# Performance work log

Hardware: AMD Instinct MI355X
Metric: run time of the kernel (lower is better)

The kernel has to match this reference:

```python
import jax, jax.numpy as jnp
import numpy as np

DIM = 512
HEADS = 8
HEAD_DIM = DIM // HEADS
SCALE = HEAD_DIM ** -0.5
CPB_HIDDEN = 512
N_CLASSES = 2
LN_EPS = 1e-5


def _layernorm(x, g, b):
    m = jnp.mean(x, axis=-1, keepdims=True)
    v = jnp.var(x, axis=-1, keepdims=True)
    return (x - m) / jnp.sqrt(v + LN_EPS) * g + b


def _coord_attention(x, coords, cpb_w1, cpb_b1, cpb_w2, cpb_b2, qkv_w, qkv_b, proj_w, proj_b):
    B, N, C = x.shape
    qkv = (x @ qkv_w + qkv_b).reshape(B, N, 3, HEADS, HEAD_DIM)
    q, k, v = jnp.moveaxis(qkv, 2, 0)  # each (B, N, H, hd)
    attn = jnp.einsum('bnhd,bmhd->bhnm', q * SCALE, k)  # (B, H, N, N)
    rel = coords[:, :, None, :] - coords[:, None, :, :]  # (B, N, N, 2)
    rel = rel / (jnp.linalg.norm(rel, axis=-1, keepdims=True) + 1e-6)
    bias = jax.nn.relu(rel @ cpb_w1 + cpb_b1) @ cpb_w2 + cpb_b2  # (B, N, N, H)
    attn = jax.nn.softmax(attn + jnp.transpose(bias, (0, 3, 1, 2)), axis=-1)
    out = jnp.einsum('bhnm,bmhd->bnhd', attn, v).reshape(B, N, C)
    return out @ proj_w + proj_b


def setup_inputs() -> dict:
    key = jax.random.key(0)
    ks = iter(jax.random.split(key, 32))
    d = {}
    d['h'] = jax.random.normal(next(ks), (1, 400, 1024), dtype=jnp.float32)
    d['coords'] = jax.random.uniform(next(ks), (1, 400, 2), dtype=jnp.float32) * 1000.0
    def lin(kw, kb, fan_in, fan_out):
        w = jax.random.normal(kw, (fan_in, fan_out), dtype=jnp.float32) / np.sqrt(fan_in)
        b = jax.random.normal(kb, (fan_out,), dtype=jnp.float32) * 0.01
        return w, b
    d['fc1_w'], d['fc1_b'] = lin(next(ks), next(ks), 1024, DIM)
    d['cls_token'] = jax.random.normal(next(ks), (1, 1, DIM), dtype=jnp.float32)
    for p in ('l1', 'l2'):
        d[p + '_norm_g'] = jnp.ones((DIM,), jnp.float32)
        d[p + '_norm_b'] = jnp.zeros((DIM,), jnp.float32)
        d[p + '_cpb_w1'], d[p + '_cpb_b1'] = lin(next(ks), next(ks), 2, CPB_HIDDEN)
        d[p + '_cpb_w2'], d[p + '_cpb_b2'] = lin(next(ks), next(ks), CPB_HIDDEN, HEADS)
        d[p + '_qkv_w'], d[p + '_qkv_b'] = lin(next(ks), next(ks), DIM, 3 * DIM)
        d[p + '_proj_w'], d[p + '_proj_b'] = lin(next(ks), next(ks), DIM, DIM)
    d['norm_g'] = jnp.ones((DIM,), jnp.float32)
    d['norm_b'] = jnp.zeros((DIM,), jnp.float32)
    d['fc2_w'], d['fc2_b'] = lin(next(ks), next(ks), DIM, N_CLASSES)
    return d


def reference(h, coords, fc1_w, fc1_b, cls_token,
              l1_norm_g, l1_norm_b, l1_cpb_w1, l1_cpb_b1, l1_cpb_w2, l1_cpb_b2,
              l1_qkv_w, l1_qkv_b, l1_proj_w, l1_proj_b,
              l2_norm_g, l2_norm_b, l2_cpb_w1, l2_cpb_b1, l2_cpb_w2, l2_cpb_b2,
              l2_qkv_w, l2_qkv_b, l2_proj_w, l2_proj_b,
              norm_g, norm_b, fc2_w, fc2_b):
    B, Np, _ = h.shape
    h = jax.nn.relu(h @ fc1_w + fc1_b)  # (B, N, 512)
    side = int(np.ceil(np.sqrt(Np)))
    add = side * side - Np  # pad bag to a perfect square (wrap-around copy)
    h = jnp.concatenate([h, h[:, :add, :]], axis=1)
    coords = jnp.concatenate([coords, coords[:, :add, :]], axis=1)
    cls = jnp.broadcast_to(cls_token, (B, 1, DIM))
    h = jnp.concatenate([cls, h], axis=1)
    coords = jnp.concatenate([jnp.zeros((B, 1, 2), h.dtype), coords], axis=1)
    h = h + _coord_attention(_layernorm(h, l1_norm_g, l1_norm_b), coords,
                             l1_cpb_w1, l1_cpb_b1, l1_cpb_w2, l1_cpb_b2,
                             l1_qkv_w, l1_qkv_b, l1_proj_w, l1_proj_b)
    h = h + _coord_attention(_layernorm(h, l2_norm_g, l2_norm_b), coords,
                             l2_cpb_w1, l2_cpb_b1, l2_cpb_w2, l2_cpb_b2,
                             l2_qkv_w, l2_qkv_b, l2_proj_w, l2_proj_b)
    h = _layernorm(h, norm_g, norm_b)[:, 0]  # CLS token
    return h @ fc2_w + fc2_b  # (B, n_classes)
```

## Files before the change

### kernel.cpp

```cpp
#include <hip/hip_runtime.h>
#include <math.h>

#define NP 401
#define DIM 512
#define LN_EPS 1e-5f
#define ATT_SCALE 0.125f
#define SP 448
#define PLANE (NP * SP)
#define CPB_M 4096
#define TSTRIDE (CPB_M + 64)
#define PQS (401L * 1536)
#define PKS (401L * 1024)
#define PVS (401L * 512)

template<bool TB, typename LA, typename LB>
__device__ __forceinline__ void gemm64(
    int kBeg, int kEnd, int tid,
    float (*as)[68], float (*bs)[68], float (&acc)[4][4],
    LA&& loadA, LB&& loadB)
{
    float aR[4], bR[4];
    loadA(kBeg, aR);
    loadB(kBeg, bR);
    for (int k0 = kBeg; k0 < kEnd; k0 += 16) {
        const int arow = tid >> 2, aq = tid & 3;
        as[aq * 4 + 0][arow] = aR[0];
        as[aq * 4 + 1][arow] = aR[1];
        as[aq * 4 + 2][arow] = aR[2];
        as[aq * 4 + 3][arow] = aR[3];
        if (!TB) {
            *(float4*)&bs[tid >> 4][(tid & 15) * 4] =
                make_float4(bR[0], bR[1], bR[2], bR[3]);
        } else {
            bs[aq * 4 + 0][arow] = bR[0];
            bs[aq * 4 + 1][arow] = bR[1];
            bs[aq * 4 + 2][arow] = bR[2];
            bs[aq * 4 + 3][arow] = bR[3];
        }
        __syncthreads();
        float nA[4] = {0.f,0.f,0.f,0.f}, nB[4] = {0.f,0.f,0.f,0.f};
        if (k0 + 16 < kEnd) { loadA(k0 + 16, nA); loadB(k0 + 16, nB); }
        const int tx = tid & 15, ty = tid >> 4;
        #pragma unroll
        for (int kk = 0; kk < 16; ++kk) {
            float4 a4 = *(const float4*)&as[kk][ty * 4];
            float4 b4 = *(const float4*)&bs[kk][tx * 4];
            float av[4] = {a4.x, a4.y, a4.z, a4.w};
            float bv[4] = {b4.x, b4.y, b4.z, b4.w};
            #pragma unroll
            for (int r = 0; r < 4; ++r)
                #pragma unroll
                for (int c = 0; c < 4; ++c)
                    acc[r][c] = fmaf(av[r], bv[c], acc[r][c]);
        }
        __syncthreads();
        #pragma unroll
        for (int j = 0; j < 4; ++j) { aR[j] = nA[j]; bR[j] = nB[j]; }
    }
}

__global__ __launch_bounds__(256) void gemm_split_kernel(
    const float* __restrict__ A, int lda,
    const float* __restrict__ B, int ldb,
    float* __restrict__ P, int ldc, long slice,
    int M, int N, int K, int skN)
{
    __shared__ float as[16][68], bs[16][68];
    const int tid = threadIdx.x;
    const int m0 = blockIdx.x * 64, n0 = blockIdx.y * 64;
    const int sk = blockIdx.z;
    const int KS = ((K + skN * 16 - 1) / (skN * 16)) * 16;
    const int kBeg = sk * KS;
    const int kEnd = (kBeg + KS < K) ? kBeg + KS : K;
    float acc[4][4] = {};

    auto loadA = [&](int k0, float r[4]) {
        r[0] = r[1] = r[2] = r[3] = 0.f;
        int gm = m0 + (tid >> 2);
        if (gm >= M) return;
        int gk = k0 + (tid & 3) * 4;
        const float* p = A + (long)gm * lda + gk;
        if (gk + 3 < kEnd) {
            float4 v = *(const float4*)p;
            r[0] = v.x; r[1] = v.y; r[2] = v.z; r[3] = v.w;
        } else {
            #pragma unroll
            for (int j = 0; j < 4; ++j) if (gk + j < kEnd) r[j] = p[j];
        }
    };
    auto loadB = [&](int k0, float r[4]) {
        r[0] = r[1] = r[2] = r[3] = 0.f;
        int gk = k0 + (tid >> 4);
        if (gk >= kEnd) return;
        int gn = n0 + (tid & 15) * 4;
        const float* p = B + (long)gk * ldb + gn;
        float4 v = *(const float4*)p;
        r[0] = v.x; r[1] = v.y; r[2] = v.z; r[3] = v.w;
    };
    if (kBeg < kEnd)
        gemm64<false>(kBeg, kEnd, tid, as, bs, acc, loadA, loadB);

    float* C = P + (long)sk * slice;
    const int tx = tid & 15, ty = tid >> 4;
    #pragma unroll
    for (int r = 0; r < 4; ++r) {
        int m = m0 + ty * 4 + r;
        if (m >= M) continue;
        *(float4*)&C[(long)m * ldc + n0 + tx * 4] =
            make_float4(acc[r][0], acc[r][1], acc[r][2], acc[r][3]);
    }
}

__global__ __launch_bounds__(256) void reduce_kernel(
    const float* __restrict__ P, long slice, int skN,
    const float* __restrict__ bias, float* __restrict__ out,
    int total, int N)
{
    int idx = (blockIdx.x * 256 + threadIdx.x) * 4;
    if (idx >= total) return;
    float4 s = *(const float4*)(P + idx);
    for (int k = 1; k < skN; ++k) {
        float4 p = *(const float4*)(P + (long)k * slice + idx);
        s.x += p.x; s.y += p.y; s.z += p.z; s.w += p.w;
    }
    if (bias) {
        const float4 b = *(const float4*)(bias + (idx % N));
        s.x += b.x; s.y += b.y; s.z += b.z; s.w += b.w;
    }
    *(float4*)(out + idx) = s;
}

__global__ __launch_bounds__(256) void qk_kernel(
    const float* __restrict__ qkv,
    const int* __restrict__ pm, const float* __restrict__ pf,
    const float* __restrict__ T, float* __restrict__ S,
    float* __restrict__ Sml)
{
    __shared__ float as[16][68], bs[16][68];
    const int tid = threadIdx.x;
    const int m0 = blockIdx.x * 64, n0 = blockIdx.y * 64, h = blockIdx.z;
    const int nb = blockIdx.y;
    float acc[4][4] = {};

    auto loadQ = [&](int k0, float r[4]) {
        int gm = m0 + (tid >> 2);
        if (gm > 400) { r[0]=r[1]=r[2]=r[3]=0.f; return; }
        int gk = k0 + (tid & 3) * 4;
        float4 v = *(const float4*)(qkv + (long)gm * 1536 + h * 64 + gk);
        r[0]=v.x; r[1]=v.y; r[2]=v.z; r[3]=v.w;
    };
    auto loadK = [&](int k0, float r[4]) {
        int gn = n0 + (tid >> 2);
        if (gn > 400) { r[0]=r[1]=r[2]=r[3]=0.f; return; }
        int gk = k0 + (tid & 3) * 4;
        float4 v = *(const float4*)(qkv + (long)gn * 1536 + 512 + h * 64 + gk);
        r[0]=v.x; r[1]=v.y; r[2]=v.z; r[3]=v.w;
    };
    gemm64<true>(0, 64, tid, as, bs, acc, loadQ, loadK);

    const int tx = tid & 15, ty = tid >> 4;
    const float* Tt = T + (long)h * TSTRIDE;
    float* Sp = S + (long)h * PLANE;
    #pragma unroll
    for (int r = 0; r < 4; ++r) {
        int i = m0 + ty * 4 + r;
        float sv[4];
        #pragma unroll
        for (int c = 0; c < 4; ++c) {
            int j = n0 + tx * 4 + c;
            if (i <= 400 && j <= 400) {
                int id = i * 416 + j;
                int mm = pm[id];
                float fr = pf[id];
                float t0 = Tt[mm], t1 = Tt[mm + 1];
                sv[c] = fmaf(acc[r][c], ATT_SCALE, fmaf(fr, t1 - t0, t0));
                Sp[(long)i * SP + j] = sv[c];
            } else {
                sv[c] = -INFINITY;
            }
        }
        float cmax = fmaxf(fmaxf(sv[0], sv[1]), fmaxf(sv[2], sv[3]));
        cmax = fmaxf(cmax, __shfl_xor(cmax, 1));
        cmax = fmaxf(cmax, __shfl_xor(cmax, 2));
        cmax = fmaxf(cmax, __shfl_xor(cmax, 4));
        cmax = fmaxf(cmax, __shfl_xor(cmax, 8));
        float cs = __expf(sv[0] - cmax) + __expf(sv[1] - cmax)
                 + __expf(sv[2] - cmax) + __expf(sv[3] - cmax);
        cs += __shfl_xor(cs, 1);
        cs += __shfl_xor(cs, 2);
        cs += __shfl_xor(cs, 4);
        cs += __shfl_xor(cs, 8);
        if (tx == 0 && i <= 400) {
            long o = ((long)(h * 401 + i) * 7 + nb) * 2;
            Sml[o] = cmax;
            Sml[o + 1] = cs;
        }
    }
}

__global__ __launch_bounds__(256) void pv_kernel(
    const float* __restrict__ S, const float* __restrict__ Sml,
    const float* __restrict__ qkv, float* __restrict__ Pv)
{
    __shared__ float as[16][68], bs[16][68];
    __shared__ float rml[64][2];
    const int tid = threadIdx.x;
    const int m0 = blockIdx.x * 64;
    const int h = blockIdx.z >> 2, sk = blockIdx.z & 3;
    const int kBeg = sk * 112;
    const int kEnd = (kBeg + 112 < NP) ? kBeg + 112 : NP;
    float acc[4][4] = {};

    if (tid < 64) {
        int row = m0 + tid;
        float M = -INFINITY, L = 0.f;
        if (row <= 400) {
            const float* q = Sml + ((long)(h * 401 + row) * 7) * 2;
            #pragma unroll
            for (int c = 0; c < 7; ++c) M = fmaxf(M, q[c * 2]);
            #pragma unroll
            for (int c = 0; c < 7; ++c) L += q[c * 2 + 1] * __expf(q[c * 2] - M);
        }
        rml[tid][0] = M;
        rml[tid][1] = (L > 0.f) ? (1.f / L) : 0.f;
    }
    __syncthreads();

    auto loadA = [&](int k0, float r[4]) {
        int gm = m0 + (tid >> 2);
        if (gm > 400) { r[0]=r[1]=r[2]=r[3]=0.f; return; }
        float M = rml[tid >> 2][0], IL = rml[tid >> 2][1];
        int gk = k0 + (tid & 3) * 4;
        const float* p = S + (long)h * PLANE + (long)gm * SP + gk;
        float t4[4] = {-INFINITY, -INFINITY, -INFINITY, -INFINITY};
        if (gk + 3 < kEnd) {
            float4 v = *(const float4*)p;
            t4[0]=v.x; t4[1]=v.y; t4[2]=v.z; t4[3]=v.w;
        } else {
            #pragma unroll
            for (int j = 0; j < 4; ++j) if (gk + j < kEnd) t4[j] = p[j];
        }
        #pragma unroll
        for (int j = 0; j < 4; ++j) r[j] = __expf(t4[j] - M) * IL;
    };
    auto loadB = [&](int k0, float r[4]) {
        r[0] = r[1] = r[2] = r[3] = 0.f;
        int key = k0 + (tid >> 4);
        if (key >= kEnd) return;
        int d = (tid & 15) * 4;
        float4 v = *(const float4*)(qkv + (long)key * 1536 + 1024 + h * 64 + d);
        r[0]=v.x; r[1]=v.y; r[2]=v.z; r[3]=v.w;
    };
    gemm64<false>(kBeg, kEnd, tid, as, bs, acc, loadA, loadB);

    float* C = Pv + (long)sk * PVS;
    const int tx = tid & 15, ty = tid >> 4;
    #pragma unroll
    for (int r = 0; r < 4; ++r) {
        int m = m0 + ty * 4 + r;
        if (m > 400) continue;
        *(float4*)&C[(long)m * 512 + h * 64 + tx * 4] =
            make_float4(acc[r][0], acc[r][1], acc[r][2], acc[r][3]);
    }
}

__global__ __launch_bounds__(256) void proj_kernel(
    const float* __restrict__ att, const float* __restrict__ projw,
    float* __restrict__ Pp)
{
    __shared__ float as[16][68], bs[16][68];
    const int tid = threadIdx.x;
    const int m0 = blockIdx.x * 64, n0 = blockIdx.y * 64, sk = blockIdx.z;
    const int kBeg = sk * 64, kEnd = kBeg + 64;
    float acc[4][4] = {};

    auto loadA = [&](int k0, float r[4]) {
        r[0] = r[1] = r[2] = r[3] = 0.f;
        int gm = m0 + (tid >> 2);
        if (gm > 400) return;
        int gk = k0 + (tid & 3) * 4;
        float4 v = *(const float4*)(att + (long)gm * 512 + gk);
        r[0]=v.x; r[1]=v.y; r[2]=v.z; r[3]=v.w;
    };
    auto loadB = [&](int k0, float r[4]) {
        int gk = k0 + (tid >> 4);
        int gn = n0 + (tid & 15) * 4;
        float4 v = *(const float4*)(projw + (long)gk * 512 + gn);
        r[0]=v.x; r[1]=v.y; r[2]=v.z; r[3]=v.w;
    };
    gemm64<false>(kBeg, kEnd, tid, as, bs, acc, loadA, loadB);

    float* C = Pp + (long)sk * PVS;
    const int tx = tid & 15, ty = tid >> 4;
    #pragma unroll
    for (int r = 0; r < 4; ++r) {
        int m = m0 + ty * 4 + r;
        if (m > 400) continue;
        *(float4*)&C[(long)m * 512 + n0 + tx * 4] =
            make_float4(acc[r][0], acc[r][1], acc[r][2], acc[r][3]);
    }
}

__global__ __launch_bounds__(256) void rowfuse_kernel(
    const float* __restrict__ P, long slice, int skN, int rowOff,
    const float* __restrict__ bias, int doRelu,
    const float* __restrict__ resid, const float* __restrict__ cls,
    float* __restrict__ h0,
    const float* __restrict__ g, const float* __restrict__ b,
    float* __restrict__ xln)
{
    const int r = blockIdx.x, t = threadIdx.x;
    float v0, v1;
    if (cls && r == 0) {
        v0 = cls[t]; v1 = cls[t + 256];
    } else {
        const float* p = P + (long)(r - rowOff) * DIM;
        v0 = bias[t]; v1 = bias[t + 256];
        for (int k = 0; k < skN; ++k) {
            v0 += p[(long)k * slice + t];
            v1 += p[(long)k * slice + t + 256];
        }
        if (resid) {
            v0 += resid[(long)r * DIM + t];
            v1 += resid[(long)r * DIM + t + 256];
        }
        if (doRelu) { v0 = fmaxf(v0, 0.f); v1 = fmaxf(v1, 0.f); }
    }
    h0[(long)r * DIM + t] = v0;
    h0[(long)r * DIM + t + 256] = v1;

    float s = v0 + v1, sq = v0 * v0 + v1 * v1;
    #pragma unroll
    for (int off = 32; off > 0; off >>= 1) {
        s += __shfl_down(s, off);
        sq += __shfl_down(sq, off);
    }
    __shared__ float ps[4], pq[4];
    int w = t >> 6, lane = t & 63;
    if (lane == 0) { ps[w] = s; pq[w] = sq; }
    __syncthreads();
    float Sm = ps[0] + ps[1] + ps[2] + ps[3];
    float Q = pq[0] + pq[1] + pq[2] + pq[3];
    float mean = Sm * (1.f / DIM);
    float var = Q * (1.f / DIM) - mean * mean;
    float inv = rsqrtf(var + LN_EPS);
    xln[(long)r * DIM + t]       = (v0 - mean) * inv * g[t] + b[t];
    xln[(long)r * DIM + t + 256] = (v1 - mean) * inv * g[t + 256] + b[t + 256];
}

__global__ __launch_bounds__(256) void cls_decode_kernel(
    const float* __restrict__ xln, const float* __restrict__ qkvw,
    const float* __restrict__ Pkv, const float* __restrict__ qkvb,
    const int* __restrict__ pm, const float* __restrict__ pf,
    const float* __restrict__ T,
    float* __restrict__ cms, float* __restrict__ cpv,
    unsigned* __restrict__ cnt)
{
    const int h = blockIdx.x, c = blockIdx.y, tid = threadIdx.x;
    const int kBeg = c * 64;
    __shared__ float q0[64], scraw[64], p[64], red[4][64], rr[2];

    if (h == 0 && c == 0 && tid == 0) *cnt = 0u;

    {
        int d = tid & 63, w4 = tid >> 6;
        const float* col = qkvw + h * 64 + d;
        float acc = 0.f;
        for (int k = w4 * 128; k < w4 * 128 + 128; ++k)
            acc = fmaf(xln[k], col[(long)k * 1536], acc);
        red[w4][d] = acc;
    }
    __syncthreads();
    if (tid < 64)
        q0[tid] = red[0][tid] + red[1][tid] + red[2][tid] + red[3][tid]
                  + qkvb[h * 64 + tid];
    __syncthreads();

    {
        int k = tid >> 2, q = tid & 3;
        int j = kBeg + k;
        float dot = 0.f;
        if (j < NP) {
            long base = (long)j * 1024 + h * 64 + q * 16;
            #pragma unroll
            for (int d = 0; d < 16; d += 4) {
                float4 x0 = *(const float4*)(Pkv + base + d);
                float4 x1 = *(const float4*)(Pkv + PKS + base + d);
                float4 x2 = *(const float4*)(Pkv + 2 * PKS + base + d);
                float4 x3 = *(const float4*)(Pkv + 3 * PKS + base + d);
                float4 bb = *(const float4*)(qkvb + 512 + h * 64 + q * 16 + d);
                float4 qq = *(const float4*)(q0 + q * 16 + d);
                dot = fmaf(qq.x, x0.x + x1.x + x2.x + x3.x + bb.x, dot);
                dot = fmaf(qq.y, x0.y + x1.y + x2.y + x3.y + bb.y, dot);
                dot = fmaf(qq.z, x0.z + x1.z + x2.z + x3.z + bb.z, dot);
                dot = fmaf(qq.w, x0.w + x1.w + x2.w + x3.w + bb.w, dot);
            }
        }
        dot += __shfl_down(dot, 2);
        dot += __shfl_down(dot, 1);
        if (q == 0) scraw[k] = dot;
    }
    __syncthreads();

    if (tid < 64) {
        int j = kBeg + tid;
        float s;
        if (j < NP) {
            int mm = pm[j];
            float fr = pf[j];
            const float* Tt = T + (long)h * TSTRIDE;
            float t0 = Tt[mm], t1 = Tt[mm + 1];
            s = fmaf(scraw[tid], ATT_SCALE, fmaf(fr, t1 - t0, t0));
        } else {
            s = -INFINITY;
        }
        float m = s;
        #pragma unroll
        for (int off = 32; off > 0; off >>= 1)
            m = fmaxf(m, __shfl_xor(m, off));
        float e = (j < NP) ? __expf(s - m) : 0.f;
        float sum = e;
        #pragma unroll
        for (int off = 32; off > 0; off >>= 1)
            sum += __shfl_xor(sum, off);
        p[tid] = e;
        if (tid == 0) { rr[0] = m; rr[1] = sum; }
    }
    __syncthreads();

    {
        int w = tid >> 6, d = tid & 63;
        float vb = qkvb[1024 + h * 64 + d];
        float acc = 0.f;
        for (int k = w; k < 64; k += 4) {
            int j = kBeg + k;
            if (j >= NP) break;
            long o = (long)j * 1024 + 512 + h * 64 + d;
            float v = Pkv[o] + Pkv[PKS + o] + Pkv[2 * PKS + o]
                      + Pkv[3 * PKS + o] + vb;
            acc = fmaf(p[k], v, acc);
        }
        red[w][d] = acc;
    }
    __syncthreads();
    if (tid < 64) {
        cpv[((long)h * 7 + c) * 64 + tid] =
            red[0][tid] + red[1][tid] + red[2][tid] + red[3][tid];
        if (tid == 0) {
            cms[(h * 7 + c) * 2 + 0] = rr[0];
            cms[(h * 7 + c) * 2 + 1] = rr[1];
        }
    }
}

__global__ __launch_bounds__(256) void cls_proj_kernel(
    const float* __restrict__ cms, const float* __restrict__ cpv,
    const float* __restrict__ projw, const float* __restrict__ projb,
    float* __restrict__ proj0,
    const float* __restrict__ h0,
    const float* __restrict__ g, const float* __restrict__ b,
    const float* __restrict__ fc2w, const float* __restrict__ fc2b,
    float* __restrict__ out, unsigned* __restrict__ cnt)
{
    __shared__ float av[512], red[4][64];
    __shared__ int isLast;
    const int bk = blockIdx.x, tid = threadIdx.x;
    for (int d = tid; d < 512; d += 256) {
        int h = d >> 6, dd = d & 63;
        float M = -INFINITY;
        #pragma unroll
        for (int c = 0; c < 7; ++c)
            M = fmaxf(M, cms[(h * 7 + c) * 2]);
        float Sx = 0.f, acc = 0.f;
        #pragma unroll
        for (int c = 0; c < 7; ++c) {
            float e = __expf(cms[(h * 7 + c) * 2] - M);
            Sx += cms[(h * 7 + c) * 2 + 1] * e;
            acc += cpv[((long)h * 7 + c) * 64 + dd] * e;
        }
        av[d] = acc / Sx;
    }
    __syncthreads();
    int gg = tid >> 6, n = bk * 64 + (tid & 63);
    float acc = 0.f;
    for (int k = gg * 128; k < gg * 128 + 128; ++k)
        acc = fmaf(av[k], projw[(long)k * 512 + n], acc);
    red[gg][tid & 63] = acc;
    __syncthreads();
    if (tid < 64)
        proj0[bk * 64 + tid] = red[0][tid] + red[1][tid] + red[2][tid]
                               + red[3][tid] + projb[bk * 64 + tid];

    __threadfence();
    if (tid == 0) isLast = (atomicAdd(cnt, 1u) == 7u);
    __syncthreads();
    if (!isLast) return;
    __threadfence();

    const int t = tid;
    float v0 = h0[t] + proj0[t];
    float v1 = h0[t + 256] + proj0[t + 256];
    float s = v0 + v1, sq = v0 * v0 + v1 * v1;
    #pragma unroll
    for (int off = 32; off > 0; off >>= 1) {
        s += __shfl_down(s, off);
        sq += __shfl_down(sq, off);
    }
    __shared__ float ps[4], pq[4], pc0[4], pc1[4];
    int w = t >> 6, lane = t & 63;
    if (lane == 0) { ps[w] = s; pq[w] = sq; }
    __syncthreads();
    float Sm = ps[0] + ps[1] + ps[2] + ps[3];
    float Q = pq[0] + pq[1] + pq[2] + pq[3];
    float mean = Sm * (1.f / DIM);
    float var = Q * (1.f / DIM) - mean * mean;
    float inv = rsqrtf(var + LN_EPS);
    float n0 = (v0 - mean) * inv * g[t] + b[t];
    float n1 = (v1 - mean) * inv * g[t + 256] + b[t + 256];
    float c0 = n0 * fc2w[t * 2]     + n1 * fc2w[(t + 256) * 2];
    float c1 = n0 * fc2w[t * 2 + 1] + n1 * fc2w[(t + 256) * 2 + 1];
    #pragma unroll
    for (int off = 32; off > 0; off >>= 1) {
        c0 += __shfl_down(c0, off);
        c1 += __shfl_down(c1, off);
    }
    if (lane == 0) { pc0[w] = c0; pc1[w] = c1; }
    __syncthreads();
    if (t == 0) {
        out[0] = pc0[0] + pc0[1] + pc0[2] + pc0[3] + fc2b[0];
        out[1] = pc1[0] + pc1[1] + pc1[2] + pc1[3] + fc2b[1];
    }
}

__global__ __launch_bounds__(256) void mega_kernel(
    const float* __restrict__ hin, const float* __restrict__ fc1_w,
    const float* __restrict__ w1_0, const float* __restrict__ b1_0,
    const float* __restrict__ w2_0, const float* __restrict__ b2_0,
    const float* __restrict__ w1_1, const float* __restrict__ b1_1,
    const float* __restrict__ w2_1, const float* __restrict__ b2_1,
    const float* __restrict__ coords,
    float* __restrict__ Pp, float* __restrict__ T,
    int* __restrict__ pm, float* __restrict__ pf)
{
    __shared__ float smem[2176];
    float (*as)[68] = (float(*)[68])smem;
    float (*bs)[68] = (float(*)[68])(smem + 1088);
    float (*red)[64][8] = (float(*)[64][8])smem;
    const int bid = blockIdx.x, tid = threadIdx.x;

    if (bid < 896) {
        int sk = bid / 56, rem = bid % 56;
        int m0 = (rem % 7) * 64, n0 = (rem / 7) * 64;
        int kBeg = sk * 64, kEnd = kBeg + 64;
        float acc[4][4] = {};
        auto loadA = [&](int k0, float r[4]) {
            r[0]=r[1]=r[2]=r[3]=0.f;
            int gm = m0 + (tid >> 2);
            if (gm >= 400) return;
            int gk = k0 + (tid & 3) * 4;
            float4 v = *(const float4*)(hin + (long)gm * 1024 + gk);
            r[0]=v.x; r[1]=v.y; r[2]=v.z; r[3]=v.w;
        };
        auto loadB = [&](int k0, float r[4]) {
            int gk = k0 + (tid >> 4);
            int gn = n0 + (tid & 15) * 4;
            float4 v = *(const float4*)(fc1_w + (long)gk * 512 + gn);
            r[0]=v.x; r[1]=v.y; r[2]=v.z; r[3]=v.w;
        };
        gemm64<false>(kBeg, kEnd, tid, as, bs, acc, loadA, loadB);
        float* C = Pp + (long)sk * PVS;
        const int tx = tid & 15, ty = tid >> 4;
        #pragma unroll
        for (int r = 0; r < 4; ++r) {
            int m = m0 + ty * 4 + r;
            if (m >= 400) continue;
            *(float4*)&C[(long)m * 512 + n0 + tx * 4] =
                make_float4(acc[r][0], acc[r][1], acc[r][2], acc[r][3]);
        }
    } else if (bid < 1026) {
        int tb = bid - 896;
        int z = tb / 65, ab = tb % 65;
        const float* w1 = z ? w1_1 : w1_0;
        const float* b1 = z ? b1_1 : b1_0;
        const float* w2 = z ? w2_1 : w2_0;
        const float* b2 = z ? b2_1 : b2_0;
        const int lane = tid & 63, wv = tid >> 6;
        float ca = 0.f, sa = 0.f;
        if (ab != 64) {
            float th = fmaf((float)(ab * 64 + lane),
                            (float)(2.0 * M_PI / CPB_M), -(float)M_PI);
            sincosf(th, &sa, &ca);
        } else if (lane == 0) {
            sincosf((float)M_PI, &sa, &ca);
        }
        float a8[8] = {};
        const int kbeg = wv * 128;
        #pragma unroll 4
        for (int k = kbeg; k < kbeg + 128; ++k) {
            float hk = fmaxf(fmaf(ca, w1[k],
                                  fmaf(sa, w1[512 + k], b1[k])), 0.f);
            #pragma unroll
            for (int h2 = 0; h2 < 8; ++h2)
                a8[h2] = fmaf(hk, w2[k * 8 + h2], a8[h2]);
        }
        #pragma unroll
        for (int h2 = 0; h2 < 8; ++h2) red[wv][lane][h2] = a8[h2];
        __syncthreads();
        if (tid < 64) {
            int aidx = ab * 64 + tid;
            if (aidx <= CPB_M + 1) {
                #pragma unroll
                for (int h2 = 0; h2 < 8; ++h2)
                    T[(long)(z * 8 + h2) * TSTRIDE + aidx] =
                        red[0][tid][h2] + red[1][tid][h2] +
                        red[2][tid][h2] + red[3][tid][h2] + b2[h2];
            }
        }
    } else {
        int p = (bid - 1026) * 256 + tid;
        if (p < NP * NP) {
            int i = p / NP, j = p - i * NP;
            float xi = (i == 0) ? 0.f : coords[(i - 1) * 2];
            float yi = (i == 0) ? 0.f : coords[(i - 1) * 2 + 1];
            float xj = (j == 0) ? 0.f : coords[(j - 1) * 2];
            float yj = (j == 0) ? 0.f : coords[(j - 1) * 2 + 1];
            float rx = xi - xj, ry = yi - yj;
            int mm; float fr;
            if (rx == 0.f && ry == 0.f) {
                mm = CPB_M + 1; fr = 0.f;
            } else {
                float x = (atan2f(ry, rx) + 3.14159265358979f)
                          * (float)(CPB_M / (2.0 * M_PI));
                int mi = (int)x;
                fr = x - (float)mi;
                mm = (mi >= CPB_M) ? mi - CPB_M : mi;
            }
            pm[i * 416 + j] = mm;
            pf[i * 416 + j] = fr;
        }
    }
}

extern "C" void kernel_launch(void* const* d_in, const int* in_sizes, int n_in,
                              void* d_out, int out_size, void* d_ws, size_t ws_size,
                              hipStream_t stream)
{
    const float* coords = (const float*)d_in[1];
    float* ws = (float*)d_ws;
    float* h0   = ws;                    ws += 401L * 512;
    float* xln  = ws;                    ws += 401L * 512;
    float* S    = ws;                    ws += 8L * PLANE;
    float* T    = ws;                    ws += 16L * TSTRIDE;
    int*   pm   = (int*)ws;              ws += 401L * 416;
    float* pf   = ws;                    ws += 401L * 416;
    float* Pq   = ws;                    ws += 4L * PQS;
    float* qkv  = ws;                    ws += 401L * 1536;
    float* Pv   = ws;                    ws += 4L * PVS;
    float* att  = ws;                    ws += 401L * 512;
    float* Pp   = ws;                    ws += 16L * PVS;
    float* proj0 = ws;                   ws += 512;
    float* cms  = ws;                    ws += 8L * 7 * 2;
    float* cpv  = ws;                    ws += 8L * 7 * 64;
    float* Sml  = ws;                    ws += 8L * 401 * 7 * 2;
    unsigned* cnt = (unsigned*)ws;       ws += 16;

    mega_kernel<<<1655, 256, 0, stream>>>(
        (const float*)d_in[0], (const float*)d_in[2],
        (const float*)d_in[7],  (const float*)d_in[8],
        (const float*)d_in[9],  (const float*)d_in[10],
        (const float*)d_in[17], (const float*)d_in[18],
        (const float*)d_in[19], (const float*)d_in[20],
        coords, Pp, T, pm, pf);

    rowfuse_kernel<<<401, 256, 0, stream>>>(
        Pp, PVS, 16, 1, (const float*)d_in[3], 1, nullptr,
        (const float*)d_in[4], h0,
        (const float*)d_in[5], (const float*)d_in[6], xln);

    gemm_split_kernel<<<dim3(7, 24, 4), 256, 0, stream>>>(
        xln, 512, (const float*)d_in[11], 1536, Pq, 1536, PQS,
        401, 1536, 512, 4);
    reduce_kernel<<<602, 256, 0, stream>>>(
        Pq, PQS, 4, (const float*)d_in[12], qkv, 401 * 1536, 1536);
    qk_kernel<<<dim3(7, 7, 8), 256, 0, stream>>>(qkv, pm, pf, T, S, Sml);
    pv_kernel<<<dim3(7, 1, 32), 256, 0, stream>>>(S, Sml, qkv, Pv);
    reduce_kernel<<<201, 256, 0, stream>>>(
        Pv, PVS, 4, nullptr, att, 401 * 512, 512);
    proj_kernel<<<dim3(7, 8, 8), 256, 0, stream>>>(
        att, (const float*)d_in[13], Pp);
    rowfuse_kernel<<<401, 256, 0, stream>>>(
        Pp, PVS, 8, 0, (const float*)d_in[14], 0, h0, nullptr, h0,
        (const float*)d_in[15], (const float*)d_in[16], xln);

    gemm_split_kernel<<<dim3(7, 16, 4), 256, 0, stream>>>(
        xln, 512, (const float*)d_in[21] + 512, 1536, Pq, 1024, PKS,
        401, 1024, 512, 4);
    cls_decode_kernel<<<dim3(8, 7), 256, 0, stream>>>(
        xln, (const float*)d_in[21], Pq, (const float*)d_in[22],
        pm, pf, T + 8L * TSTRIDE, cms, cpv, cnt);
    cls_proj_kernel<<<8, 256, 0, stream>>>(
        cms, cpv, (const float*)d_in[23], (const float*)d_in[24], proj0,
        h0, (const float*)d_in[25], (const float*)d_in[26],
        (const float*)d_in[27], (const float*)d_in[28], (float*)d_out, cnt);
}
```

Before: 244.1 us.

## Fuse QK, softmax and PV into split-key flash kernel, combine in proj

Merges the score, softmax and PV stages into one kernel per (query tile, key tile, head). It computes local exp-probabilities and multiplies them by the V tile in shared memory, writing per-key-block partial outputs with their row max and sum. The projection kernel then rescales and sums the seven partials while loading its A operand. This removes the full score-plane write and read, the separate PV kernel and a reduce launch. In exchange the projection kernel reads seven partial outputs per element, with some redundant reads across column tiles.

```diff
diff --git a/kernel.cpp b/kernel.cpp
--- a/kernel.cpp
+++ b/kernel.cpp
@@ -5,8 +5,6 @@
 #define DIM 512
 #define LN_EPS 1e-5f
 #define ATT_SCALE 0.125f
-#define SP 448
-#define PLANE (NP * SP)
 #define CPB_M 4096
 #define TSTRIDE (CPB_M + 64)
 #define PQS (401L * 1536)
@@ -130,17 +128,39 @@
     *(float4*)(out + idx) = s;
 }
 
-__global__ __launch_bounds__(256) void qk_kernel(
+__global__ __launch_bounds__(256) void flash_kernel(
     const float* __restrict__ qkv,
     const int* __restrict__ pm, const float* __restrict__ pf,
-    const float* __restrict__ T, float* __restrict__ S,
-    float* __restrict__ Sml)
+    const float* __restrict__ T,
+    float* __restrict__ PO,
+    float* __restrict__ Pml)
 {
     __shared__ float as[16][68], bs[16][68];
+    __shared__ float pT[64][68];
+    __shared__ float vs[64][68];
     const int tid = threadIdx.x;
-    const int m0 = blockIdx.x * 64, n0 = blockIdx.y * 64, h = blockIdx.z;
-    const int nb = blockIdx.y;
+    const int m0 = blockIdx.x * 64, nb = blockIdx.y, h = blockIdx.z;
+    const int n0 = nb * 64;
     float acc[4][4] = {};
+
+    float vreg[4][4];
+    {
+        int key = n0 + (tid >> 2);
+        int d0 = (tid & 3) * 16;
+        if (key <= 400) {
+            const float* p = qkv + (long)key * 1536 + 1024 + h * 64 + d0;
+            #pragma unroll
+            for (int i = 0; i < 4; ++i) {
+                float4 v = *(const float4*)(p + i * 4);
+                vreg[i][0] = v.x; vreg[i][1] = v.y;
+                vreg[i][2] = v.z; vreg[i][3] = v.w;
+            }
+        } else {
+            #pragma unroll
+            for (int i = 0; i < 4; ++i)
+                vreg[i][0] = vreg[i][1] = vreg[i][2] = vreg[i][3] = 0.f;
+        }
+    }
 
     auto loadQ = [&](int k0, float r[4]) {
         int gm = m0 + (tid >> 2);
@@ -158,9 +178,17 @@
     };
     gemm64<true>(0, 64, tid, as, bs, acc, loadQ, loadK);
 
+    {
+        int key = tid >> 2, d0 = (tid & 3) * 16;
+        #pragma unroll
+        for (int i = 0; i < 4; ++i)
+            *(float4*)&vs[key][d0 + i * 4] =
+                make_float4(vreg[i][0], vreg[i][1], vreg[i][2], vreg[i][3]);
+    }
+
     const int tx = tid & 15, ty = tid >> 4;
     const float* Tt = T + (long)h * TSTRIDE;
-    float* Sp = S + (long)h * PLANE;
+    float p[4][4];
     #pragma unroll
     for (int r = 0; r < 4; ++r) {
         int i = m0 + ty * 4 + r;
@@ -174,7 +202,6 @@
                 float fr = pf[id];
                 float t0 = Tt[mm], t1 = Tt[mm + 1];
                 sv[c] = fmaf(acc[r][c], ATT_SCALE, fmaf(fr, t1 - t0, t0));
-                Sp[(long)i * SP + j] = sv[c];
             } else {
                 sv[c] = -INFINITY;
             }
@@ -184,103 +211,96 @@
         cmax = fmaxf(cmax, __shfl_xor(cmax, 2));
         cmax = fmaxf(cmax, __shfl_xor(cmax, 4));
         cmax = fmaxf(cmax, __shfl_xor(cmax, 8));
-        float cs = __expf(sv[0] - cmax) + __expf(sv[1] - cmax)
-                 + __expf(sv[2] - cmax) + __expf(sv[3] - cmax);
+        const bool rowok = (i <= 400);
+        #pragma unroll
+        for (int c = 0; c < 4; ++c)
+            p[r][c] = rowok ? __expf(sv[c] - cmax) : 0.f;
+        float cs = p[r][0] + p[r][1] + p[r][2] + p[r][3];
         cs += __shfl_xor(cs, 1);
         cs += __shfl_xor(cs, 2);
         cs += __shfl_xor(cs, 4);
         cs += __shfl_xor(cs, 8);
-        if (tx == 0 && i <= 400) {
+        if (tx == 0 && rowok) {
             long o = ((long)(h * 401 + i) * 7 + nb) * 2;
-            Sml[o] = cmax;
-            Sml[o + 1] = cs;
-        }
-    }
-}
-
-__global__ __launch_bounds__(256) void pv_kernel(
-    const float* __restrict__ S, const float* __restrict__ Sml,
-    const float* __restrict__ qkv, float* __restrict__ Pv)
-{
-    __shared__ float as[16][68], bs[16][68];
-    __shared__ float rml[64][2];
-    const int tid = threadIdx.x;
-    const int m0 = blockIdx.x * 64;
-    const int h = blockIdx.z >> 2, sk = blockIdx.z & 3;
-    const int kBeg = sk * 112;
-    const int kEnd = (kBeg + 112 < NP) ? kBeg + 112 : NP;
-    float acc[4][4] = {};
-
-    if (tid < 64) {
-        int row = m0 + tid;
-        float M = -INFINITY, L = 0.f;
-        if (row <= 400) {
-            const float* q = Sml + ((long)(h * 401 + row) * 7) * 2;
-            #pragma unroll
-            for (int c = 0; c < 7; ++c) M = fmaxf(M, q[c * 2]);
-            #pragma unroll
-            for (int c = 0; c < 7; ++c) L += q[c * 2 + 1] * __expf(q[c * 2] - M);
-        }
-        rml[tid][0] = M;
-        rml[tid][1] = (L > 0.f) ? (1.f / L) : 0.f;
-    }
-    __syncthreads();
-
-    auto loadA = [&](int k0, float r[4]) {
-        int gm = m0 + (tid >> 2);
-        if (gm > 400) { r[0]=r[1]=r[2]=r[3]=0.f; return; }
-        float M = rml[tid >> 2][0], IL = rml[tid >> 2][1];
-        int gk = k0 + (tid & 3) * 4;
-        const float* p = S + (long)h * PLANE + (long)gm * SP + gk;
-        float t4[4] = {-INFINITY, -INFINITY, -INFINITY, -INFINITY};
-        if (gk + 3 < kEnd) {
-            float4 v = *(const float4*)p;
-            t4[0]=v.x; t4[1]=v.y; t4[2]=v.z; t4[3]=v.w;
-        } else {
-            #pragma unroll
-            for (int j = 0; j < 4; ++j) if (gk + j < kEnd) t4[j] = p[j];
-        }
-        #pragma unroll
-        for (int j = 0; j < 4; ++j) r[j] = __expf(t4[j] - M) * IL;
-    };
-    auto loadB = [&](int k0, float r[4]) {
-        r[0] = r[1] = r[2] = r[3] = 0.f;
-        int key = k0 + (tid >> 4);
-        if (key >= kEnd) return;
-        int d = (tid & 15) * 4;
-        float4 v = *(const float4*)(qkv + (long)key * 1536 + 1024 + h * 64 + d);
-        r[0]=v.x; r[1]=v.y; r[2]=v.z; r[3]=v.w;
-    };
-    gemm64<false>(kBeg, kEnd, tid, as, bs, acc, loadA, loadB);
-
-    float* C = Pv + (long)sk * PVS;
-    const int tx = tid & 15, ty = tid >> 4;
+            Pml[o] = cmax;
+            Pml[o + 1] = cs;
+        }
+    }
+    #pragma unroll
+    for (int c = 0; c < 4; ++c)
+        *(float4*)&pT[tx * 4 + c][ty * 4] =
+            make_float4(p[0][c], p[1][c], p[2][c], p[3][c]);
+    __syncthreads();
+
+    float o[4][4] = {};
+    #pragma unroll 16
+    for (int kk = 0; kk < 64; ++kk) {
+        float4 a4 = *(const float4*)&pT[kk][ty * 4];
+        float4 b4 = *(const float4*)&vs[kk][tx * 4];
+        float av[4] = {a4.x, a4.y, a4.z, a4.w};
+        float bv[4] = {b4.x, b4.y, b4.z, b4.w};
+        #pragma unroll
+        for (int r = 0; r < 4; ++r)
+            #pragma unroll
+            for (int c = 0; c < 4; ++c)
+                o[r][c] = fmaf(av[r], bv[c], o[r][c]);
+    }
+
+    float* C = PO + (long)nb * PVS;
     #pragma unroll
     for (int r = 0; r < 4; ++r) {
         int m = m0 + ty * 4 + r;
         if (m > 400) continue;
         *(float4*)&C[(long)m * 512 + h * 64 + tx * 4] =
-            make_float4(acc[r][0], acc[r][1], acc[r][2], acc[r][3]);
+            make_float4(o[r][0], o[r][1], o[r][2], o[r][3]);
     }
 }
 
 __global__ __launch_bounds__(256) void proj_kernel(
-    const float* __restrict__ att, const float* __restrict__ projw,
-    float* __restrict__ Pp)
+    const float* __restrict__ PO, const float* __restrict__ Pml,
+    const float* __restrict__ projw, float* __restrict__ Pp)
 {
     __shared__ float as[16][68], bs[16][68];
+    __shared__ float wls[64][8];
     const int tid = threadIdx.x;
     const int m0 = blockIdx.x * 64, n0 = blockIdx.y * 64, sk = blockIdx.z;
     const int kBeg = sk * 64, kEnd = kBeg + 64;
     float acc[4][4] = {};
 
-    auto loadA = [&](int k0, float r[4]) {
-        r[0] = r[1] = r[2] = r[3] = 0.f;
-        int gm = m0 + (tid >> 2);
+    if (tid < 64) {
+        int row = m0 + tid;
+        if (row <= 400) {
+            const float* q = Pml + ((long)(sk * 401 + row) * 7) * 2;
+            float M = -INFINITY;
+            #pragma unroll
+            for (int c = 0; c < 7; ++c) M = fmaxf(M, q[c * 2]);
+            float D = 0.f;
+            #pragma unroll
+            for (int c = 0; c < 7; ++c) D += q[c * 2 + 1] * __expf(q[c * 2] - M);
+            float iD = 1.f / D;
+            #pragma unroll
+            for (int c = 0; c < 7; ++c) wls[tid][c] = __expf(q[c * 2] - M) * iD;
+        } else {
+            #pragma unroll
+            for (int c = 0; c < 7; ++c) wls[tid][c] = 0.f;
+        }
+    }
+    __syncthreads();
+
+    auto loadA = [&](int k0, float r4[4]) {
+        r4[0] = r4[1] = r4[2] = r4[3] = 0.f;
+        int lm = tid >> 2, gm = m0 + lm;
         if (gm > 400) return;
         int gk = k0 + (tid & 3) * 4;
-        float4 v = *(const float4*)(att + (long)gm * 512 + gk);
-        r[0]=v.x; r[1]=v.y; r[2]=v.z; r[3]=v.w;
+        #pragma unroll
+        for (int s = 0; s < 7; ++s) {
+            float4 v = *(const float4*)(PO + (long)s * PVS + (long)gm * 512 + gk);
+            float w = wls[lm][s];
+            r4[0] = fmaf(w, v.x, r4[0]);
+            r4[1] = fmaf(w, v.y, r4[1]);
+            r4[2] = fmaf(w, v.z, r4[2]);
+            r4[3] = fmaf(w, v.w, r4[3]);
+        }
     };
     auto loadB = [&](int k0, float r[4]) {
         int gk = k0 + (tid >> 4);
@@ -649,19 +669,17 @@
     float* ws = (float*)d_ws;
     float* h0   = ws;                    ws += 401L * 512;
     float* xln  = ws;                    ws += 401L * 512;
-    float* S    = ws;                    ws += 8L * PLANE;
+    float* PO   = ws;                    ws += 7L * PVS;
     float* T    = ws;                    ws += 16L * TSTRIDE;
     int*   pm   = (int*)ws;              ws += 401L * 416;
     float* pf   = ws;                    ws += 401L * 416;
     float* Pq   = ws;                    ws += 4L * PQS;
     float* qkv  = ws;                    ws += 401L * 1536;
-    float* Pv   = ws;                    ws += 4L * PVS;
-    float* att  = ws;                    ws += 401L * 512;
     float* Pp   = ws;                    ws += 16L * PVS;
     float* proj0 = ws;                   ws += 512;
     float* cms  = ws;                    ws += 8L * 7 * 2;
     float* cpv  = ws;                    ws += 8L * 7 * 64;
-    float* Sml  = ws;                    ws += 8L * 401 * 7 * 2;
+    float* Pml  = ws;                    ws += 8L * 401 * 7 * 2;
     unsigned* cnt = (unsigned*)ws;       ws += 16;
 
     mega_kernel<<<1655, 256, 0, stream>>>(
@@ -682,12 +700,10 @@
         401, 1536, 512, 4);
     reduce_kernel<<<602, 256, 0, stream>>>(
         Pq, PQS, 4, (const float*)d_in[12], qkv, 401 * 1536, 1536);
-    qk_kernel<<<dim3(7, 7, 8), 256, 0, stream>>>(qkv, pm, pf, T, S, Sml);
-    pv_kernel<<<dim3(7, 1, 32), 256, 0, stream>>>(S, Sml, qkv, Pv);
-    reduce_kernel<<<201, 256, 0, stream>>>(
-        Pv, PVS, 4, nullptr, att, 401 * 512, 512);
+    flash_kernel<<<dim3(7, 7, 8), 256, 0, stream>>>(
+        qkv, pm, pf, T, PO, Pml);
     proj_kernel<<<dim3(7, 8, 8), 256, 0, stream>>>(
-        att, (const float*)d_in[13], Pp);
+        PO, Pml, (const float*)d_in[13], Pp);
     rowfuse_kernel<<<401, 256, 0, stream>>>(
         Pp, PVS, 8, 0, (const float*)d_in[14], 0, h0, nullptr, h0,
         (const float*)d_in[15], (const float*)d_in[16], xln);
```

Measured after the change: 241.3 us. Within noise of the previous version (-1.2%).
